# Kernel tuning notes

Measured on AMD Instinct MI355X. Metric: run time of the kernel, lower is better.

The kernel has to match this reference:

```python
import jax, jax.numpy as jnp
import numpy as np

N_QUBITS = 12
FAST_DEPTH = 4
FAST_DECAY = 0.9
LATENT = 512
BATCH = 2048


def _apply_ry(state, theta, wire):
    # state: (B, 2**n) real; RY is a real rotation. PennyLane default.qubit:
    # wire 0 is the most-significant bit of the state index.
    B = state.shape[0]
    s = state.reshape(B, 1 << wire, 2, -1)
    h = theta * 0.5
    c = jnp.cos(h)[:, None, None]
    sn = jnp.sin(h)[:, None, None]
    s0, s1 = s[:, :, 0], s[:, :, 1]
    out = jnp.stack([c * s0 - sn * s1, sn * s0 + c * s1], axis=2)
    return out.reshape(state.shape)


def _apply_cnot_adjacent(state, wire):
    # CNOT with control=wire, target=wire+1 (nearest-neighbor chain)
    B = state.shape[0]
    s = state.reshape(B, 1 << wire, 2, 2, -1)
    out = jnp.stack([s[:, :, 0], s[:, :, 1, ::-1]], axis=2)
    return out.reshape(state.shape)


def _fwp_circuit(x, fast, n_qubits, n_outputs):
    # x: (B, n_qubits) RY encoding angles; fast: (B, depth, n_qubits)
    B = x.shape[0]
    dim = 1 << n_qubits
    # Hadamard layer on |0...0> -> uniform positive real amplitudes.
    state = jnp.full((B, dim), 2.0 ** (-n_qubits / 2), dtype=x.dtype)
    for w in range(n_qubits):
        state = _apply_ry(state, x[:, w], w)
    for layer in range(fast.shape[1]):
        for w in range(n_qubits - 1):
            state = _apply_cnot_adjacent(state, w)
        for w in range(n_qubits):
            state = _apply_ry(state, fast[:, layer, w], w)
    probs = state * state  # real state -> |amp|^2
    outs = []
    for w in range(n_outputs):
        p = probs.reshape(B, 1 << w, 2, -1)
        outs.append(p[:, :, 0].sum(axis=(1, 2)) - p[:, :, 1].sum(axis=(1, 2)))
    return jnp.stack(outs, axis=1)  # (B, n_outputs) PauliZ expvals


def setup_inputs() -> dict:
    key = jax.random.key(0)
    ks = jax.random.split(key, 6)
    n, depth, latent = N_QUBITS, FAST_DEPTH, LATENT
    return {
        "x_t": jax.random.normal(ks[0], (BATCH, n), jnp.float32),
        "fast_prev": jax.random.normal(ks[1], (BATCH, depth, n), jnp.float32) * 0.1,
        "W_enc": jax.random.normal(ks[2], (latent, n), jnp.float32) / np.sqrt(n).astype(np.float32),
        "b_enc": jnp.zeros((latent,), jnp.float32),
        "W_upd": jax.random.normal(ks[3], (depth * n, latent), jnp.float32) / np.sqrt(latent).astype(np.float32),
        "b_upd": jnp.zeros((depth * n,), jnp.float32),
        "W_ro": jax.random.normal(ks[4], (1, n), jnp.float32) / np.sqrt(n).astype(np.float32),
        "b_ro": jnp.zeros((1,), jnp.float32),
    }


def reference(x_t, fast_prev, W_enc, b_enc, W_upd, b_upd, W_ro, b_ro):
    latent = jnp.tanh(x_t @ W_enc.T + b_enc)
    delta = (latent @ W_upd.T + b_upd).reshape(x_t.shape[0], FAST_DEPTH, N_QUBITS)
    fast_next = FAST_DECAY * fast_prev + delta
    q_out = _fwp_circuit(x_t, fast_next, N_QUBITS, N_QUBITS)  # n_outputs = n_qubits
    y_t = q_out @ W_ro.T + b_ro
    return (y_t, fast_next)
```

## Files before the change

kernel.cpp:

```cpp
#include <hip/hip_runtime.h>

static constexpr int NQ    = 12;
static constexpr int DEPTH = 4;
static constexpr int LAT   = 512;
static constexpr int FAST  = DEPTH * NQ;
static constexpr float DECAY = 0.9f;
static constexpr int P     = 68;

using v2f = __attribute__((ext_vector_type(2))) float;


template<int S, int B>
__device__ __forceinline__ void bfly_half(float (&v)[64], float c, float s) {
    v2f c2 = {c, c}, s2 = {s, s};
    #pragma unroll
    for (int r0 = B; r0 < B + 32; r0 += 2) {
        if ((r0 & S) == 0) {
            v2f a = {v[r0],     v[r0 + 1]};
            v2f b = {v[r0 + S], v[r0 + S + 1]};
            v2f na = c2 * a - s2 * b;
            v2f nb = s2 * a + c2 * b;
            v[r0]     = na.x;  v[r0 + 1]     = na.y;
            v[r0 + S] = nb.x;  v[r0 + S + 1] = nb.y;
        }
    }
}

template<int B>
__device__ __forceinline__ void bfly1_half(float (&v)[64], float c, float s) {
    v2f cs = {c, s}, nsc = {-s, c};
    #pragma unroll
    for (int r0 = B; r0 < B + 32; r0 += 2) {
        float a = v[r0], b = v[r0 + 1];
        v2f aa = {a, a}, bb = {b, b};
        v2f res = cs * aa + nsc * bb;
        v[r0]     = res.x;
        v[r0 + 1] = res.y;
    }
}

template<int B>
__device__ __forceinline__ void ry5_half(float (&v)[64], const v2f* cs) {
    bfly_half<16, B>(v, cs[0].x, cs[0].y);
    bfly_half<8,  B>(v, cs[1].x, cs[1].y);
    bfly_half<4,  B>(v, cs[2].x, cs[2].y);
    bfly_half<2,  B>(v, cs[3].x, cs[3].y);
    bfly1_half<B>(v, cs[4].x, cs[4].y);
}

__device__ __forceinline__ void bfly32(float (&v)[64], float c, float s) {
    v2f c2 = {c, c}, s2 = {s, s};
    #pragma unroll
    for (int r0 = 0; r0 < 32; r0 += 2) {
        v2f a = {v[r0],      v[r0 + 1]};
        v2f b = {v[r0 + 32], v[r0 + 33]};
        v2f na = c2 * a - s2 * b;
        v2f nb = s2 * a + c2 * b;
        v[r0]      = na.x;  v[r0 + 1]  = na.y;
        v[r0 + 32] = nb.x;  v[r0 + 33] = nb.y;
    }
}

__device__ __forceinline__ void ry6(float (&v)[64], const v2f* cs) {
    ry5_half<0>(v, cs + 1);
    ry5_half<32>(v, cs + 1);
    bfly32(v, cs[0].x, cs[0].y);
}

__device__ __forceinline__ void p1w(const float (&v)[64], float* X, int lane) {
    #pragma unroll
    for (int k = 0; k < 16; k++)
        *(float4*)&X[lane * P + 4 * k] =
            (float4){v[4 * k], v[4 * k + 1], v[4 * k + 2], v[4 * k + 3]};
}
__device__ __forceinline__ void p1r(float (&v)[64], const float* X, int A0, int A1) {
    #pragma unroll
    for (int r = 0; r < 64; r++) {
        const int g = r ^ (r >> 1);
        v[r] = X[g * P + ((r & 1) ? A1 : A0)];
    }
}
__device__ __forceinline__ void p2w(const float (&v)[64], float* X, int lane) {
    #pragma unroll
    for (int q = 0; q < 64; q++) X[q * P + lane] = v[q];
}
__device__ __forceinline__ void p2r(float (&v)[64], const float* X, int lane) {
    #pragma unroll
    for (int k = 0; k < 16; k++) {
        float4 t = *(const float4*)&X[lane * P + 4 * k];
        v[4 * k]     = t.x;  v[4 * k + 1] = t.y;
        v[4 * k + 2] = t.z;  v[4 * k + 3] = t.w;
    }
}

__device__ __forceinline__ void init_state(float (&v)[64], const float (&xa)[NQ], int lane) {
    float g0[NQ], g1[NQ];
    #pragma unroll
    for (int w = 0; w < NQ; w++) {
        float hh = 0.5f * xa[w];
        float c = __cosf(hh), s = __sinf(hh);
        g0[w] = (c - s) * 0.70710678118654752f;
        g1[w] = (c + s) * 0.70710678118654752f;
    }
    float L = 1.0f;
    #pragma unroll
    for (int w = 0; w < 6; w++)
        L *= ((lane >> (5 - w)) & 1) ? g1[w] : g0[w];
    v[0] = L;
    #pragma unroll
    for (int w = 6; w < NQ; w++) {
        const int S = 1 << (11 - w);
        #pragma unroll
        for (int r = 0; r < 64; r += 2 * S) {
            v[r + S] = v[r] * g1[w];
            v[r]     = v[r] * g0[w];
        }
    }
}

__global__ __launch_bounds__(64, 1)
void fwp_kernel(const float* __restrict__ x_t,
                const float* __restrict__ fast_prev,
                const float* __restrict__ W_enc,
                const float* __restrict__ b_enc,
                const float* __restrict__ W_upd,
                const float* __restrict__ b_upd,
                const float* __restrict__ W_ro,
                const float* __restrict__ b_ro,
                float* __restrict__ out_y,
                float* __restrict__ out_fast) {
    const int lane = threadIdx.x;
    const int eA   = 2 * blockIdx.x;
    const int eB   = eA + 1;

    __shared__ __align__(16) float XA[64 * P];
    __shared__ __align__(16) float XB[64 * P];
    __shared__ __align__(8)  v2f   csA[FAST], csB[FAST];

    float* latA = XA;
    float* latB = XB;

    float xaA[NQ], xaB[NQ];
    #pragma unroll
    for (int k = 0; k < NQ; k++) {
        xaA[k] = x_t[eA * NQ + k];
        xaB[k] = x_t[eB * NQ + k];
    }

    {
        const float4* we = (const float4*)(W_enc + lane * 8 * NQ);
        float4 be0 = *(const float4*)&b_enc[8 * lane];
        float4 be1 = *(const float4*)&b_enc[8 * lane + 4];
        float be[8] = {be0.x, be0.y, be0.z, be0.w, be1.x, be1.y, be1.z, be1.w};
        float lA[8], lB[8];
        #pragma unroll
        for (int t = 0; t < 8; t++) {
            float4 a0 = we[3 * t], a1 = we[3 * t + 1], a2 = we[3 * t + 2];
            float sA = be[t]
                + a0.x * xaA[0] + a0.y * xaA[1] + a0.z * xaA[2]  + a0.w * xaA[3]
                + a1.x * xaA[4] + a1.y * xaA[5] + a1.z * xaA[6]  + a1.w * xaA[7]
                + a2.x * xaA[8] + a2.y * xaA[9] + a2.z * xaA[10] + a2.w * xaA[11];
            float sB = be[t]
                + a0.x * xaB[0] + a0.y * xaB[1] + a0.z * xaB[2]  + a0.w * xaB[3]
                + a1.x * xaB[4] + a1.y * xaB[5] + a1.z * xaB[6]  + a1.w * xaB[7]
                + a2.x * xaB[8] + a2.y * xaB[9] + a2.z * xaB[10] + a2.w * xaB[11];
            lA[t] = tanhf(sA);
            lB[t] = tanhf(sB);
        }
        *(float4*)&latA[8 * lane]     = (float4){lA[0], lA[1], lA[2], lA[3]};
        *(float4*)&latA[8 * lane + 4] = (float4){lA[4], lA[5], lA[6], lA[7]};
        *(float4*)&latB[8 * lane]     = (float4){lB[0], lB[1], lB[2], lB[3]};
        *(float4*)&latB[8 * lane + 4] = (float4){lB[4], lB[5], lB[6], lB[7]};
    }

    if (lane < FAST) {
        const float4* wr = (const float4*)(W_upd + lane * LAT);
        const float4* la = (const float4*)(latA);
        const float4* lb = (const float4*)(latB);
        float base = b_upd[lane];
        float sA = base, sB = base;
        #pragma unroll 8
        for (int j = 0; j < LAT / 4; j++) {
            float4 w4 = wr[j];
            float4 a4 = la[j];
            float4 b4 = lb[j];
            sA += w4.x * a4.x + w4.y * a4.y + w4.z * a4.z + w4.w * a4.w;
            sB += w4.x * b4.x + w4.y * b4.y + w4.z * b4.z + w4.w * b4.w;
        }
        float angA = DECAY * fast_prev[eA * FAST + lane] + sA;
        float angB = DECAY * fast_prev[eB * FAST + lane] + sB;
        out_fast[eA * FAST + lane] = angA;
        out_fast[eB * FAST + lane] = angB;
        csA[lane] = (v2f){__cosf(0.5f * angA), __sinf(0.5f * angA)};
        csB[lane] = (v2f){__cosf(0.5f * angB), __sinf(0.5f * angB)};
    }

    float vA[64], vB[64];
    init_state(vA, xaA, lane);
    init_state(vB, xaB, lane);

    const int A0 = ((lane ^ (lane >> 1)) & 31) | (lane & 32);
    const int A1 = A0 ^ 32;

    #pragma unroll 1
    for (int layer = 0; layer < DEPTH; layer++) {
        v2f ca[NQ], cb[NQ];
        #pragma unroll
        for (int w = 0; w < NQ; w++) {
            ca[w] = csA[layer * NQ + w];
            cb[w] = csB[layer * NQ + w];
        }

        p1w(vA, XA, lane);
        p1w(vB, XB, lane);
        p1r(vA, XA, A0, A1);
        p1r(vB, XB, A0, A1);
        ry6(vA, ca);
        ry6(vB, cb);

        p2w(vA, XA, lane);
        p2w(vB, XB, lane);
        p2r(vA, XA, lane);
        p2r(vB, XB, lane);
        ry6(vA, ca + 6);
        ry6(vB, cb + 6);
    }

    float wro[NQ];
    #pragma unroll
    for (int w = 0; w < NQ; w++) wro[w] = W_ro[w];
    float sl = 0.0f;
    #pragma unroll
    for (int w = 0; w < 6; w++)
        sl += ((lane >> (5 - w)) & 1) ? -wro[w] : wro[w];

    float totA = 0.0f, pwA[6] = {0,0,0,0,0,0};
    float totB = 0.0f, pwB[6] = {0,0,0,0,0,0};
    #pragma unroll
    for (int r = 0; r < 64; r++) {
        float pA = vA[r] * vA[r];
        float pB = vB[r] * vB[r];
        totA += pA;  totB += pB;
        pwA[0] += (r & 32) ? -pA : pA;  pwB[0] += (r & 32) ? -pB : pB;
        pwA[1] += (r & 16) ? -pA : pA;  pwB[1] += (r & 16) ? -pB : pB;
        pwA[2] += (r & 8)  ? -pA : pA;  pwB[2] += (r & 8)  ? -pB : pB;
        pwA[3] += (r & 4)  ? -pA : pA;  pwB[3] += (r & 4)  ? -pB : pB;
        pwA[4] += (r & 2)  ? -pA : pA;  pwB[4] += (r & 2)  ? -pB : pB;
        pwA[5] += (r & 1)  ? -pA : pA;  pwB[5] += (r & 1)  ? -pB : pB;
    }
    float yA = sl * totA, yB = sl * totB;
    #pragma unroll
    for (int k = 0; k < 6; k++) {
        yA += wro[6 + k] * pwA[k];
        yB += wro[6 + k] * pwB[k];
    }
    #pragma unroll
    for (int m = 32; m >= 1; m >>= 1) {
        yA += __shfl_xor(yA, m, 64);
        yB += __shfl_xor(yB, m, 64);
    }
    if (lane == 0) {
        float br = b_ro[0];
        out_y[eA] = yA + br;
        out_y[eB] = yB + br;
    }
}

extern "C" void kernel_launch(void* const* d_in, const int* in_sizes, int n_in,
                              void* d_out, int out_size, void* d_ws, size_t ws_size,
                              hipStream_t stream) {
    const float* x_t       = (const float*)d_in[0];
    const float* fast_prev = (const float*)d_in[1];
    const float* W_enc     = (const float*)d_in[2];
    const float* b_enc     = (const float*)d_in[3];
    const float* W_upd     = (const float*)d_in[4];
    const float* b_upd     = (const float*)d_in[5];
    const float* W_ro      = (const float*)d_in[6];
    const float* b_ro      = (const float*)d_in[7];
    float* out = (float*)d_out;

    fwp_kernel<<<1024, 64, 0, stream>>>(x_t, fast_prev, W_enc, b_enc,
                                        W_upd, b_upd, W_ro, b_ro,
                                        out , out + 2048 );
}
```

Measured before the change: 106.7 us.

## Replace LDS transposes with DPP lane exchanges and Gray-coded register layout

Drops one of the two shared-memory transposes per layer. Five of the lane-indexed wires now rotate by exchanging values between lanes with DPP moves and ds_swizzle, and the register-indexed wires use a Gray-coded in-register layout so the CNOT chain becomes a fixed relabeling. The remaining LDS round trip applies the top wire's rotation as the data is read back, and the A and B work is interleaved to overlap LDS latency. The cost is 64 extra DPP moves per lane wire and more register pressure from the tmp array and permutations.

```diff
diff --git a/kernel.cpp b/kernel.cpp
--- a/kernel.cpp
+++ b/kernel.cpp
@@ -10,87 +10,79 @@
 using v2f = __attribute__((ext_vector_type(2))) float;
 
 
-template<int S, int B>
-__device__ __forceinline__ void bfly_half(float (&v)[64], float c, float s) {
-    v2f c2 = {c, c}, s2 = {s, s};
-    #pragma unroll
-    for (int r0 = B; r0 < B + 32; r0 += 2) {
-        if ((r0 & S) == 0) {
-            v2f a = {v[r0],     v[r0 + 1]};
-            v2f b = {v[r0 + S], v[r0 + S + 1]};
-            v2f na = c2 * a - s2 * b;
-            v2f nb = s2 * a + c2 * b;
-            v[r0]     = na.x;  v[r0 + 1]     = na.y;
-            v[r0 + S] = nb.x;  v[r0 + S + 1] = nb.y;
-        }
-    }
+__device__ __forceinline__ constexpr int G6(int x)  { return (x ^ (x >> 1)) & 63; }
+__device__ __forceinline__ constexpr int GINV(int x){ int y = x; y ^= y >> 1; y ^= y >> 2; y ^= y >> 4; return y & 63; }
+
+template<int CTRL>
+__device__ __forceinline__ float dppf(float x){
+    return __int_as_float(__builtin_amdgcn_mov_dpp(__float_as_int(x), CTRL, 0xF, 0xF, false));
+}
+template<int B> __device__ __forceinline__ float lexch(float x);
+template<> __device__ __forceinline__ float lexch<0>(float x){ return dppf<0xB1>(x); }
+template<> __device__ __forceinline__ float lexch<1>(float x){ return dppf<0x4E>(x); }
+template<> __device__ __forceinline__ float lexch<2>(float x){ return dppf<0x141>(dppf<0x1B>(x)); }
+template<> __device__ __forceinline__ float lexch<3>(float x){ return dppf<0x128>(x); }
+template<> __device__ __forceinline__ float lexch<4>(float x){
+    return __int_as_float(__builtin_amdgcn_ds_swizzle(__float_as_int(x), 0x401F));
 }
 
 template<int B>
-__device__ __forceinline__ void bfly1_half(float (&v)[64], float c, float s) {
-    v2f cs = {c, s}, nsc = {-s, c};
-    #pragma unroll
-    for (int r0 = B; r0 < B + 32; r0 += 2) {
-        float a = v[r0], b = v[r0 + 1];
-        v2f aa = {a, a}, bb = {b, b};
-        v2f res = cs * aa + nsc * bb;
-        v[r0]     = res.x;
-        v[r0 + 1] = res.y;
+__device__ __forceinline__ void lanewire(float (&t)[64], float c, float ss){
+    #pragma unroll
+    for (int k = 0; k < 64; k++){
+        float p = lexch<B>(t[k]);
+        t[k] = __builtin_fmaf(c, t[k], ss * p);
     }
 }
 
 template<int B>
-__device__ __forceinline__ void ry5_half(float (&v)[64], const v2f* cs) {
-    bfly_half<16, B>(v, cs[0].x, cs[0].y);
-    bfly_half<8,  B>(v, cs[1].x, cs[1].y);
-    bfly_half<4,  B>(v, cs[2].x, cs[2].y);
-    bfly_half<2,  B>(v, cs[3].x, cs[3].y);
-    bfly1_half<B>(v, cs[4].x, cs[4].y);
-}
-
-__device__ __forceinline__ void bfly32(float (&v)[64], float c, float s) {
-    v2f c2 = {c, c}, s2 = {s, s};
-    #pragma unroll
-    for (int r0 = 0; r0 < 32; r0 += 2) {
-        v2f a = {v[r0],      v[r0 + 1]};
-        v2f b = {v[r0 + 32], v[r0 + 33]};
-        v2f na = c2 * a - s2 * b;
-        v2f nb = s2 * a + c2 * b;
-        v[r0]      = na.x;  v[r0 + 1]  = na.y;
-        v[r0 + 32] = nb.x;  v[r0 + 33] = nb.y;
-    }
-}
-
-__device__ __forceinline__ void ry6(float (&v)[64], const v2f* cs) {
-    ry5_half<0>(v, cs + 1);
-    ry5_half<32>(v, cs + 1);
-    bfly32(v, cs[0].x, cs[0].y);
-}
-
-__device__ __forceinline__ void p1w(const float (&v)[64], float* X, int lane) {
-    #pragma unroll
-    for (int k = 0; k < 16; k++)
-        *(float4*)&X[lane * P + 4 * k] =
-            (float4){v[4 * k], v[4 * k + 1], v[4 * k + 2], v[4 * k + 3]};
-}
-__device__ __forceinline__ void p1r(float (&v)[64], const float* X, int A0, int A1) {
-    #pragma unroll
-    for (int r = 0; r < 64; r++) {
-        const int g = r ^ (r >> 1);
-        v[r] = X[g * P + ((r & 1) ? A1 : A0)];
-    }
-}
-__device__ __forceinline__ void p2w(const float (&v)[64], float* X, int lane) {
-    #pragma unroll
-    for (int q = 0; q < 64; q++) X[q * P + lane] = v[q];
-}
-__device__ __forceinline__ void p2r(float (&v)[64], const float* X, int lane) {
-    #pragma unroll
-    for (int k = 0; k < 16; k++) {
-        float4 t = *(const float4*)&X[lane * P + 4 * k];
-        v[4 * k]     = t.x;  v[4 * k + 1] = t.y;
-        v[4 * k + 2] = t.z;  v[4 * k + 3] = t.w;
-    }
+__device__ __forceinline__ void regwire(float (&t)[64], float c, float s){
+    constexpr int M = (B == 0) ? 1 : ((1 << B) | (1 << (B - 1)));
+    #pragma unroll
+    for (int k = 0; k < 64; k++){
+        if (__builtin_parity((unsigned)(k >> B)) == 0){
+            float a = t[k], b = t[k ^ M];
+            t[k]     = c * a - s * b;
+            t[k ^ M] = s * a + c * b;
+        }
+    }
+}
+
+__device__ __forceinline__ void stageW(const float (&t)[64], float* X, int wbase){
+    #pragma unroll
+    for (int m = 0; m < 16; m++)
+        *(float4*)&X[wbase + 4*m] =
+            (float4){ t[G6(4*m+0)], t[G6(4*m+1)], t[G6(4*m+2)], t[G6(4*m+3)] };
+}
+
+__device__ __forceinline__ void stageR0(float (&t)[64], const float* X, int rs, int rp, int off,
+                                        float c0, float ss0){
+    #pragma unroll
+    for (int m = 0; m < 16; m++){
+        int col = (4*m) ^ off;
+        float4 a = *(const float4*)&X[rs + col];
+        float4 b = *(const float4*)&X[rp + col];
+        t[4*m+0] = __builtin_fmaf(c0, a.x, ss0 * b.x);
+        t[4*m+1] = __builtin_fmaf(c0, a.y, ss0 * b.y);
+        t[4*m+2] = __builtin_fmaf(c0, a.z, ss0 * b.z);
+        t[4*m+3] = __builtin_fmaf(c0, a.w, ss0 * b.w);
+    }
+}
+
+__device__ __forceinline__ void wiresLane(float (&t)[64], const v2f* c, int lane){
+    { v2f cs = c[1]; lanewire<4>(t, cs.x, (lane & 16) ? cs.y : -cs.y); }
+    { v2f cs = c[2]; lanewire<3>(t, cs.x, (lane &  8) ? cs.y : -cs.y); }
+    { v2f cs = c[3]; lanewire<2>(t, cs.x, (lane &  4) ? cs.y : -cs.y); }
+    { v2f cs = c[4]; lanewire<1>(t, cs.x, (lane &  2) ? cs.y : -cs.y); }
+    { v2f cs = c[5]; lanewire<0>(t, cs.x, (lane &  1) ? cs.y : -cs.y); }
+}
+__device__ __forceinline__ void wiresReg(float (&t)[64], const v2f* c){
+    { v2f cs = c[6];  regwire<5>(t, cs.x, cs.y); }
+    { v2f cs = c[7];  regwire<4>(t, cs.x, cs.y); }
+    { v2f cs = c[8];  regwire<3>(t, cs.x, cs.y); }
+    { v2f cs = c[9];  regwire<2>(t, cs.x, cs.y); }
+    { v2f cs = c[10]; regwire<1>(t, cs.x, cs.y); }
+    { v2f cs = c[11]; regwire<0>(t, cs.x, cs.y); }
 }
 
 __device__ __forceinline__ void init_state(float (&v)[64], const float (&xa)[NQ], int lane) {
@@ -195,35 +187,36 @@
         csB[lane] = (v2f){__cosf(0.5f * angB), __sinf(0.5f * angB)};
     }
 
-    float vA[64], vB[64];
-    init_state(vA, xaA, lane);
-    init_state(vB, xaB, lane);
-
-    const int A0 = ((lane ^ (lane >> 1)) & 31) | (lane & 32);
-    const int A1 = A0 ^ 32;
+    float tmp[64], tA[64], tB[64];
+    init_state(tmp, xaA, lane);
+    #pragma unroll
+    for (int k = 0; k < 64; k++) tA[k] = tmp[GINV(k)];
+    init_state(tmp, xaB, lane);
+    #pragma unroll
+    for (int k = 0; k < 64; k++) tB[k] = tmp[GINV(k)];
+
+    const int wbase = lane * P;
+    const int gl    = (lane ^ (lane >> 1)) & 63;
+    const int rs    = gl * P;
+    const int rp    = (gl ^ 48) * P;
+    const int off   = (lane & 1) * 32;
 
     #pragma unroll 1
     for (int layer = 0; layer < DEPTH; layer++) {
-        v2f ca[NQ], cb[NQ];
-        #pragma unroll
-        for (int w = 0; w < NQ; w++) {
-            ca[w] = csA[layer * NQ + w];
-            cb[w] = csB[layer * NQ + w];
-        }
-
-        p1w(vA, XA, lane);
-        p1w(vB, XB, lane);
-        p1r(vA, XA, A0, A1);
-        p1r(vB, XB, A0, A1);
-        ry6(vA, ca);
-        ry6(vB, cb);
-
-        p2w(vA, XA, lane);
-        p2w(vB, XB, lane);
-        p2r(vA, XA, lane);
-        p2r(vB, XB, lane);
-        ry6(vA, ca + 6);
-        ry6(vB, cb + 6);
+        const v2f* cA = csA + layer * NQ;
+        const v2f* cB = csB + layer * NQ;
+        v2f a0 = cA[0], b0 = cB[0];
+        float ssA0 = (lane & 32) ? a0.y : -a0.y;
+        float ssB0 = (lane & 32) ? b0.y : -b0.y;
+
+        stageW(tA, XA, wbase);
+        stageR0(tA, XA, rs, rp, off, a0.x, ssA0);
+        stageW(tB, XB, wbase);
+        wiresLane(tA, cA, lane);
+        stageR0(tB, XB, rs, rp, off, b0.x, ssB0);
+        wiresReg(tA, cA);
+        wiresLane(tB, cB, lane);
+        wiresReg(tB, cB);
     }
 
     float wro[NQ];
@@ -238,8 +231,9 @@
     float totB = 0.0f, pwB[6] = {0,0,0,0,0,0};
     #pragma unroll
     for (int r = 0; r < 64; r++) {
-        float pA = vA[r] * vA[r];
-        float pB = vB[r] * vB[r];
+        float aA = tA[G6(r)], aB = tB[G6(r)];
+        float pA = aA * aA;
+        float pB = aB * aB;
         totA += pA;  totB += pB;
         pwA[0] += (r & 32) ? -pA : pA;  pwB[0] += (r & 32) ? -pB : pB;
         pwA[1] += (r & 16) ? -pA : pA;  pwB[1] += (r & 16) ? -pB : pB;
```

New measurement: 121.6 us. 1.14x slower.

## Replace LDS transposes with cross-lane permutes and DPP butterflies for lane-qubit gates

Applied to the files above, without the earlier changes.

The state layout changes so that lane bits hold the high qubits and register bits hold the low qubits. Each layer no longer does two shared-memory transposes. It applies the CNOT chain through a ds_bpermute gather and runs the six lane-qubit RY gates as cross-lane butterflies using bpermute, ds_swizzle and DPP moves, followed by the register-local ry6. This drops the large LDS staging buffers and their write/read round trips. The cost is many more per-element cross-lane ops (64 per gate per state), plus a temporary 64-register array per state, which raises register pressure.

```diff
diff --git a/kernel.cpp b/kernel.cpp
--- a/kernel.cpp
+++ b/kernel.cpp
@@ -5,10 +5,22 @@
 static constexpr int LAT   = 512;
 static constexpr int FAST  = DEPTH * NQ;
 static constexpr float DECAY = 0.9f;
-static constexpr int P     = 68;
 
 using v2f = __attribute__((ext_vector_type(2))) float;
 
+
+__device__ __forceinline__ constexpr int G6(int x)  { return (x ^ (x >> 1)) & 63; }
+
+__device__ __forceinline__ float bperm(int idx, float v){
+    return __int_as_float(__builtin_amdgcn_ds_bpermute(idx, __float_as_int(v)));
+}
+template<int CTRL>
+__device__ __forceinline__ float dppf(float x){
+    return __int_as_float(__builtin_amdgcn_mov_dpp(__float_as_int(x), CTRL, 0xF, 0xF, false));
+}
+__device__ __forceinline__ float swz16(float x){
+    return __int_as_float(__builtin_amdgcn_ds_swizzle(__float_as_int(x), 0x401F));
+}
 
 template<int S, int B>
 __device__ __forceinline__ void bfly_half(float (&v)[64], float c, float s) {
@@ -25,7 +37,6 @@
         }
     }
 }
-
 template<int B>
 __device__ __forceinline__ void bfly1_half(float (&v)[64], float c, float s) {
     v2f cs = {c, s}, nsc = {-s, c};
@@ -38,7 +49,6 @@
         v[r0 + 1] = res.y;
     }
 }
-
 template<int B>
 __device__ __forceinline__ void ry5_half(float (&v)[64], const v2f* cs) {
     bfly_half<16, B>(v, cs[0].x, cs[0].y);
@@ -47,7 +57,6 @@
     bfly_half<2,  B>(v, cs[3].x, cs[3].y);
     bfly1_half<B>(v, cs[4].x, cs[4].y);
 }
-
 __device__ __forceinline__ void bfly32(float (&v)[64], float c, float s) {
     v2f c2 = {c, c}, s2 = {s, s};
     #pragma unroll
@@ -60,37 +69,10 @@
         v[r0 + 32] = nb.x;  v[r0 + 33] = nb.y;
     }
 }
-
 __device__ __forceinline__ void ry6(float (&v)[64], const v2f* cs) {
     ry5_half<0>(v, cs + 1);
     ry5_half<32>(v, cs + 1);
     bfly32(v, cs[0].x, cs[0].y);
-}
-
-__device__ __forceinline__ void p1w(const float (&v)[64], float* X, int lane) {
-    #pragma unroll
-    for (int k = 0; k < 16; k++)
-        *(float4*)&X[lane * P + 4 * k] =
-            (float4){v[4 * k], v[4 * k + 1], v[4 * k + 2], v[4 * k + 3]};
-}
-__device__ __forceinline__ void p1r(float (&v)[64], const float* X, int A0, int A1) {
-    #pragma unroll
-    for (int r = 0; r < 64; r++) {
-        const int g = r ^ (r >> 1);
-        v[r] = X[g * P + ((r & 1) ? A1 : A0)];
-    }
-}
-__device__ __forceinline__ void p2w(const float (&v)[64], float* X, int lane) {
-    #pragma unroll
-    for (int q = 0; q < 64; q++) X[q * P + lane] = v[q];
-}
-__device__ __forceinline__ void p2r(float (&v)[64], const float* X, int lane) {
-    #pragma unroll
-    for (int k = 0; k < 16; k++) {
-        float4 t = *(const float4*)&X[lane * P + 4 * k];
-        v[4 * k]     = t.x;  v[4 * k + 1] = t.y;
-        v[4 * k + 2] = t.z;  v[4 * k + 3] = t.w;
-    }
 }
 
 __device__ __forceinline__ void init_state(float (&v)[64], const float (&xa)[NQ], int lane) {
@@ -104,12 +86,12 @@
     }
     float L = 1.0f;
     #pragma unroll
-    for (int w = 0; w < 6; w++)
-        L *= ((lane >> (5 - w)) & 1) ? g1[w] : g0[w];
+    for (int w = 6; w < NQ; w++)
+        L *= ((lane >> (11 - w)) & 1) ? g1[w] : g0[w];
     v[0] = L;
     #pragma unroll
-    for (int w = 6; w < NQ; w++) {
-        const int S = 1 << (11 - w);
+    for (int w = 0; w < 6; w++) {
+        const int S = 32 >> w;
         #pragma unroll
         for (int r = 0; r < 64; r += 2 * S) {
             v[r + S] = v[r] * g1[w];
@@ -133,12 +115,8 @@
     const int eA   = 2 * blockIdx.x;
     const int eB   = eA + 1;
 
-    __shared__ __align__(16) float XA[64 * P];
-    __shared__ __align__(16) float XB[64 * P];
+    __shared__ __align__(16) float latA[LAT], latB[LAT];
     __shared__ __align__(8)  v2f   csA[FAST], csB[FAST];
-
-    float* latA = XA;
-    float* latB = XB;
 
     float xaA[NQ], xaB[NQ];
     #pragma unroll
@@ -195,35 +173,102 @@
         csB[lane] = (v2f){__cosf(0.5f * angB), __sinf(0.5f * angB)};
     }
 
-    float vA[64], vB[64];
-    init_state(vA, xaA, lane);
-    init_state(vB, xaB, lane);
-
-    const int A0 = ((lane ^ (lane >> 1)) & 31) | (lane & 32);
-    const int A1 = A0 ^ 32;
+    float xA[64], xB[64];
+    init_state(xA, xaA, lane);
+    init_state(xB, xaB, lane);
+
+    const int idxA  = G6(lane) * 4;
+    const int idxB  = idxA ^ 128;
+    const int idx32 = (lane * 4) ^ 128;
 
     #pragma unroll 1
     for (int layer = 0; layer < DEPTH; layer++) {
-        v2f ca[NQ], cb[NQ];
+        v2f cA[NQ], cB[NQ];
         #pragma unroll
         for (int w = 0; w < NQ; w++) {
-            ca[w] = csA[layer * NQ + w];
-            cb[w] = csB[layer * NQ + w];
-        }
-
-        p1w(vA, XA, lane);
-        p1w(vB, XB, lane);
-        p1r(vA, XA, A0, A1);
-        p1r(vB, XB, A0, A1);
-        ry6(vA, ca);
-        ry6(vB, cb);
-
-        p2w(vA, XA, lane);
-        p2w(vB, XB, lane);
-        p2r(vA, XA, lane);
-        p2r(vB, XB, lane);
-        ry6(vA, ca + 6);
-        ry6(vB, cb + 6);
+            cA[w] = csA[layer * NQ + w];
+            cB[w] = csB[layer * NQ + w];
+        }
+
+        float tA[64], tB[64];
+        #pragma unroll
+        for (int h = 0; h < 64; h++) {
+            const int g   = G6(h);
+            const int idx = (h & 1) ? idxB : idxA;
+            tA[h] = bperm(idx, xA[g]);
+            tB[h] = bperm(idx, xB[g]);
+        }
+        #pragma unroll
+        for (int h = 0; h < 64; h++) { xA[h] = tA[h]; xB[h] = tB[h]; }
+
+        {
+            float sa = (lane & 32) ? cA[6].y : -cA[6].y;
+            float sb = (lane & 32) ? cB[6].y : -cB[6].y;
+            #pragma unroll
+            for (int h = 0; h < 64; h++) {
+                float pa = bperm(idx32, xA[h]);
+                float pb = bperm(idx32, xB[h]);
+                xA[h] = __builtin_fmaf(cA[6].x, xA[h], sa * pa);
+                xB[h] = __builtin_fmaf(cB[6].x, xB[h], sb * pb);
+            }
+        }
+        {
+            float sa = (lane & 16) ? cA[7].y : -cA[7].y;
+            float sb = (lane & 16) ? cB[7].y : -cB[7].y;
+            #pragma unroll
+            for (int h = 0; h < 64; h++) {
+                float pa = swz16(xA[h]);
+                float pb = swz16(xB[h]);
+                xA[h] = __builtin_fmaf(cA[7].x, xA[h], sa * pa);
+                xB[h] = __builtin_fmaf(cB[7].x, xB[h], sb * pb);
+            }
+        }
+        {
+            float sa = (lane & 8) ? cA[8].y : -cA[8].y;
+            float sb = (lane & 8) ? cB[8].y : -cB[8].y;
+            #pragma unroll
+            for (int h = 0; h < 64; h++) {
+                float pa = dppf<0x128>(xA[h]);
+                float pb = dppf<0x128>(xB[h]);
+                xA[h] = __builtin_fmaf(cA[8].x, xA[h], sa * pa);
+                xB[h] = __builtin_fmaf(cB[8].x, xB[h], sb * pb);
+            }
+        }
+        {
+            float sa = (lane & 4) ? cA[9].y : -cA[9].y;
+            float sb = (lane & 4) ? cB[9].y : -cB[9].y;
+            #pragma unroll
+            for (int h = 0; h < 64; h++) {
+                float pa = dppf<0x141>(dppf<0x1B>(xA[h]));
+                float pb = dppf<0x141>(dppf<0x1B>(xB[h]));
+                xA[h] = __builtin_fmaf(cA[9].x, xA[h], sa * pa);
+                xB[h] = __builtin_fmaf(cB[9].x, xB[h], sb * pb);
+            }
+        }
+        {
+            float sa = (lane & 2) ? cA[10].y : -cA[10].y;
+            float sb = (lane & 2) ? cB[10].y : -cB[10].y;
+            #pragma unroll
+            for (int h = 0; h < 64; h++) {
+                float pa = dppf<0x4E>(xA[h]);
+                float pb = dppf<0x4E>(xB[h]);
+                xA[h] = __builtin_fmaf(cA[10].x, xA[h], sa * pa);
+                xB[h] = __builtin_fmaf(cB[10].x, xB[h], sb * pb);
+            }
+        }
+        {
+            float sa = (lane & 1) ? cA[11].y : -cA[11].y;
+            float sb = (lane & 1) ? cB[11].y : -cB[11].y;
+            #pragma unroll
+            for (int h = 0; h < 64; h++) {
+                float pa = dppf<0xB1>(xA[h]);
+                float pb = dppf<0xB1>(xB[h]);
+                xA[h] = __builtin_fmaf(cA[11].x, xA[h], sa * pa);
+                xB[h] = __builtin_fmaf(cB[11].x, xB[h], sb * pb);
+            }
+        }
+        ry6(xA, cA);
+        ry6(xB, cB);
     }
 
     float wro[NQ];
@@ -231,15 +276,15 @@
     for (int w = 0; w < NQ; w++) wro[w] = W_ro[w];
     float sl = 0.0f;
     #pragma unroll
-    for (int w = 0; w < 6; w++)
-        sl += ((lane >> (5 - w)) & 1) ? -wro[w] : wro[w];
+    for (int w = 6; w < NQ; w++)
+        sl += ((lane >> (11 - w)) & 1) ? -wro[w] : wro[w];
 
     float totA = 0.0f, pwA[6] = {0,0,0,0,0,0};
     float totB = 0.0f, pwB[6] = {0,0,0,0,0,0};
     #pragma unroll
     for (int r = 0; r < 64; r++) {
-        float pA = vA[r] * vA[r];
-        float pB = vB[r] * vB[r];
+        float pA = xA[r] * xA[r];
+        float pB = xB[r] * xB[r];
         totA += pA;  totB += pB;
         pwA[0] += (r & 32) ? -pA : pA;  pwB[0] += (r & 32) ? -pB : pB;
         pwA[1] += (r & 16) ? -pA : pA;  pwB[1] += (r & 16) ? -pB : pB;
@@ -251,8 +296,8 @@
     float yA = sl * totA, yB = sl * totB;
     #pragma unroll
     for (int k = 0; k < 6; k++) {
-        yA += wro[6 + k] * pwA[k];
-        yB += wro[6 + k] * pwB[k];
+        yA += wro[k] * pwA[k];
+        yB += wro[k] * pwB[k];
     }
     #pragma unroll
     for (int m = 32; m >= 1; m >>= 1) {
```

Result: slower. 115.3 us (+8.0%).

## Apply last-layer low-wire rotations via cross-lane permutes instead of LDS transpose

Applied to the files above, without the earlier changes.

For the final circuit layer, the second LDS transpose (p2w/p2r) is replaced by doing the rotations on wires 6-11 in the lane dimension, using permlane32/16 swaps and DPP moves. The readout mapping of wires to lane bits and register bits is swapped to match the resulting layout. The kernel also moves init_state ahead of the matvec and splits the W_upd dot product into four accumulators to expose more ILP. This removes one round of LDS writes, reads and waits per element pair. In exchange it adds many cross-lane ops (64 per wire per state) and relies on gfx950-specific permlane swap instructions.

```diff
diff --git a/kernel.cpp b/kernel.cpp
--- a/kernel.cpp
+++ b/kernel.cpp
@@ -91,6 +91,21 @@
         v[4 * k]     = t.x;  v[4 * k + 1] = t.y;
         v[4 * k + 2] = t.z;  v[4 * k + 3] = t.w;
     }
+}
+
+template<int CTRL>
+__device__ __forceinline__ float dppf(float x){
+    return __int_as_float(__builtin_amdgcn_mov_dpp(__float_as_int(x), CTRL, 0xF, 0xF, false));
+}
+__device__ __forceinline__ float xsum32(float x){
+    float a = x, b = x;
+    asm("v_permlane32_swap_b32 %0, %1" : "+v"(a), "+v"(b));
+    return a + b;
+}
+__device__ __forceinline__ float xsum16(float x){
+    float a = x, b = x;
+    asm("v_permlane16_swap_b32 %0, %1" : "+v"(a), "+v"(b));
+    return a + b;
 }
 
 __device__ __forceinline__ void init_state(float (&v)[64], const float (&xa)[NQ], int lane) {
@@ -146,6 +161,10 @@
         xaA[k] = x_t[eA * NQ + k];
         xaB[k] = x_t[eB * NQ + k];
     }
+
+    float vA[64], vB[64];
+    init_state(vA, xaA, lane);
+    init_state(vB, xaB, lane);
 
     {
         const float4* we = (const float4*)(W_enc + lane * 8 * NQ);
@@ -177,16 +196,25 @@
         const float4* wr = (const float4*)(W_upd + lane * LAT);
         const float4* la = (const float4*)(latA);
         const float4* lb = (const float4*)(latB);
+        float a0s = 0.f, a1s = 0.f, a2s = 0.f, a3s = 0.f;
+        float b0s = 0.f, b1s = 0.f, b2s = 0.f, b3s = 0.f;
+        #pragma unroll 4
+        for (int j = 0; j < LAT / 4; j += 4) {
+            float4 w0 = wr[j],     w1 = wr[j + 1], w2 = wr[j + 2], w3 = wr[j + 3];
+            float4 p0 = la[j],     p1 = la[j + 1], p2 = la[j + 2], p3 = la[j + 3];
+            float4 q0 = lb[j],     q1 = lb[j + 1], q2 = lb[j + 2], q3 = lb[j + 3];
+            a0s += w0.x * p0.x + w0.y * p0.y + w0.z * p0.z + w0.w * p0.w;
+            a1s += w1.x * p1.x + w1.y * p1.y + w1.z * p1.z + w1.w * p1.w;
+            a2s += w2.x * p2.x + w2.y * p2.y + w2.z * p2.z + w2.w * p2.w;
+            a3s += w3.x * p3.x + w3.y * p3.y + w3.z * p3.z + w3.w * p3.w;
+            b0s += w0.x * q0.x + w0.y * q0.y + w0.z * q0.z + w0.w * q0.w;
+            b1s += w1.x * q1.x + w1.y * q1.y + w1.z * q1.z + w1.w * q1.w;
+            b2s += w2.x * q2.x + w2.y * q2.y + w2.z * q2.z + w2.w * q2.w;
+            b3s += w3.x * q3.x + w3.y * q3.y + w3.z * q3.z + w3.w * q3.w;
+        }
         float base = b_upd[lane];
-        float sA = base, sB = base;
-        #pragma unroll 8
-        for (int j = 0; j < LAT / 4; j++) {
-            float4 w4 = wr[j];
-            float4 a4 = la[j];
-            float4 b4 = lb[j];
-            sA += w4.x * a4.x + w4.y * a4.y + w4.z * a4.z + w4.w * a4.w;
-            sB += w4.x * b4.x + w4.y * b4.y + w4.z * b4.z + w4.w * b4.w;
-        }
+        float sA = base + ((a0s + a1s) + (a2s + a3s));
+        float sB = base + ((b0s + b1s) + (b2s + b3s));
         float angA = DECAY * fast_prev[eA * FAST + lane] + sA;
         float angB = DECAY * fast_prev[eB * FAST + lane] + sB;
         out_fast[eA * FAST + lane] = angA;
@@ -195,15 +223,13 @@
         csB[lane] = (v2f){__cosf(0.5f * angB), __sinf(0.5f * angB)};
     }
 
-    float vA[64], vB[64];
-    init_state(vA, xaA, lane);
-    init_state(vB, xaB, lane);
-
     const int A0 = ((lane ^ (lane >> 1)) & 31) | (lane & 32);
     const int A1 = A0 ^ 32;
 
+    v2f caL[NQ], cbL[NQ];
+
     #pragma unroll 1
-    for (int layer = 0; layer < DEPTH; layer++) {
+    for (int layer = 0; layer < DEPTH - 1; layer++) {
         v2f ca[NQ], cb[NQ];
         #pragma unroll
         for (int w = 0; w < NQ; w++) {
@@ -226,13 +252,84 @@
         ry6(vB, cb + 6);
     }
 
+    {
+        #pragma unroll
+        for (int w = 0; w < NQ; w++) {
+            caL[w] = csA[(DEPTH - 1) * NQ + w];
+            cbL[w] = csB[(DEPTH - 1) * NQ + w];
+        }
+        p1w(vA, XA, lane);
+        p1w(vB, XB, lane);
+        p1r(vA, XA, A0, A1);
+        p1r(vB, XB, A0, A1);
+        ry6(vA, caL);
+        ry6(vB, cbL);
+
+        {
+            float svA = (lane & 32) ? caL[6].y : -caL[6].y;
+            float svB = (lane & 32) ? cbL[6].y : -cbL[6].y;
+            float cmA = caL[6].x - svA, cmB = cbL[6].x - svB;
+            #pragma unroll
+            for (int h = 0; h < 64; h++) {
+                vA[h] = __builtin_fmaf(cmA, vA[h], svA * xsum32(vA[h]));
+                vB[h] = __builtin_fmaf(cmB, vB[h], svB * xsum32(vB[h]));
+            }
+        }
+        {
+            float svA = (lane & 16) ? caL[7].y : -caL[7].y;
+            float svB = (lane & 16) ? cbL[7].y : -cbL[7].y;
+            float cmA = caL[7].x - svA, cmB = cbL[7].x - svB;
+            #pragma unroll
+            for (int h = 0; h < 64; h++) {
+                vA[h] = __builtin_fmaf(cmA, vA[h], svA * xsum16(vA[h]));
+                vB[h] = __builtin_fmaf(cmB, vB[h], svB * xsum16(vB[h]));
+            }
+        }
+        {
+            float svA = (lane & 8) ? caL[8].y : -caL[8].y;
+            float svB = (lane & 8) ? cbL[8].y : -cbL[8].y;
+            #pragma unroll
+            for (int h = 0; h < 64; h++) {
+                vA[h] = __builtin_fmaf(caL[8].x, vA[h], svA * dppf<0x128>(vA[h]));
+                vB[h] = __builtin_fmaf(cbL[8].x, vB[h], svB * dppf<0x128>(vB[h]));
+            }
+        }
+        {
+            float svA = (lane & 4) ? caL[9].y : -caL[9].y;
+            float svB = (lane & 4) ? cbL[9].y : -cbL[9].y;
+            #pragma unroll
+            for (int h = 0; h < 64; h++) {
+                vA[h] = __builtin_fmaf(caL[9].x, vA[h], svA * dppf<0x141>(dppf<0x1B>(vA[h])));
+                vB[h] = __builtin_fmaf(cbL[9].x, vB[h], svB * dppf<0x141>(dppf<0x1B>(vB[h])));
+            }
+        }
+        {
+            float svA = (lane & 2) ? caL[10].y : -caL[10].y;
+            float svB = (lane & 2) ? cbL[10].y : -cbL[10].y;
+            #pragma unroll
+            for (int h = 0; h < 64; h++) {
+                vA[h] = __builtin_fmaf(caL[10].x, vA[h], svA * dppf<0x4E>(vA[h]));
+                vB[h] = __builtin_fmaf(cbL[10].x, vB[h], svB * dppf<0x4E>(vB[h]));
+            }
+        }
+        {
+            float svA = (lane & 1) ? caL[11].y : -caL[11].y;
+            float svB = (lane & 1) ? cbL[11].y : -cbL[11].y;
+            #pragma unroll
+            for (int h = 0; h < 64; h++) {
+                vA[h] = __builtin_fmaf(caL[11].x, vA[h], svA * dppf<0xB1>(vA[h]));
+                vB[h] = __builtin_fmaf(cbL[11].x, vB[h], svB * dppf<0xB1>(vB[h]));
+            }
+        }
+    }
+
     float wro[NQ];
     #pragma unroll
     for (int w = 0; w < NQ; w++) wro[w] = W_ro[w];
     float sl = 0.0f;
     #pragma unroll
-    for (int w = 0; w < 6; w++)
-        sl += ((lane >> (5 - w)) & 1) ? -wro[w] : wro[w];
+    for (int w = 6; w < NQ; w++)
+        sl += ((lane >> (11 - w)) & 1) ? -wro[w] : wro[w];
 
     float totA = 0.0f, pwA[6] = {0,0,0,0,0,0};
     float totB = 0.0f, pwB[6] = {0,0,0,0,0,0};
@@ -251,8 +348,8 @@
     float yA = sl * totA, yB = sl * totB;
     #pragma unroll
     for (int k = 0; k < 6; k++) {
-        yA += wro[6 + k] * pwA[k];
-        yB += wro[6 + k] * pwB[k];
+        yA += wro[k] * pwA[k];
+        yB += wro[k] * pwB[k];
     }
     #pragma unroll
     for (int m = 32; m >= 1; m >>= 1) {
```

New measurement: 112.3 us. +5.3%, slower.
